# Kernel optimization log

Hardware: AMD Instinct MI355X
Metric: run time of the kernel (lower is better)

Reference implementation:

```python
import jax, jax.numpy as jnp
import numpy as np

RADIUS = 5
KS = 2 * RADIUS - 1          # kernel_size = 9
PAD = KS // 2                # 4
CENTER = RADIUS - 1          # 4 (== PAD)
EPS = 1e-10


def _offsets_and_kernel():
    # Distance kernel exactly as torch.meshgrid(indexing='ij') in the module;
    # the center entry is skipped in the loop, so drop it here.
    yy, xx = np.meshgrid(np.arange(KS), np.arange(KS), indexing='ij')
    dist = np.sqrt((xx - CENTER) ** 2 + (yy - CENTER) ** 2).astype(np.float32)
    keep = ~((yy == CENTER) & (xx == CENTER))
    return (yy[keep].astype(np.int32), xx[keep].astype(np.int32), dist[keep])


def setup_inputs() -> dict:
    key = jax.random.key(0)
    target = (jax.random.uniform(key, (5, 2048, 2048)) < 0.15).astype(jnp.float32)
    return {"target": target}


def reference(target):
    # target: [5, H, W] binary float masks
    H, W = target.shape[1], target.shape[2]
    feature_weight = jnp.sum(target, axis=0)                      # [H, W]
    combined = (feature_weight > 0).astype(jnp.float32)           # [H, W]

    padded = jnp.pad(combined, PAD, mode='edge')                  # replicate pad
    oi, oj, kv = _offsets_and_kernel()
    offs = (jnp.asarray(oi), jnp.asarray(oj), jnp.asarray(kv))

    def body(min_d, off):
        i, j, k = off
        shifted = jax.lax.dynamic_slice(padded, (i, j), (H, W))
        diff = (shifted != combined).astype(jnp.float32)
        d = jnp.where(diff > 0, k / (diff + EPS), jnp.inf)
        return jnp.minimum(min_d, d), None

    min_d, _ = jax.lax.scan(body, jnp.full((H, W), jnp.inf, jnp.float32), offs)

    contour = jnp.where(jnp.isfinite(min_d), 1.0 / (min_d + EPS), 0.0)
    w = (feature_weight + contour) ** 2
    w = (w - w.min()) / (w.max() - w.min() + EPS)
    return w * combined
```

## Files before the change

kernel.cpp:

```cpp
#include <hip/hip_runtime.h>
#include <math.h>
#include <utility>

static constexpr int HH = 2048;
static constexpr int WW = 2048;
static constexpr int NPIX = HH * WW;
static constexpr int WPR32 = WW / 32;
static constexpr int HPR = WW / 16;

template <typename F, int... Is>
__device__ __forceinline__ void sf_impl(F&& f, std::integer_sequence<int, Is...>) {
    (f(std::integral_constant<int, Is>{}), ...);
}
template <int N, typename F>
__device__ __forceinline__ void static_for(F&& f) {
    sf_impl(f, std::make_integer_sequence<int, N>{});
}

__host__ __device__ constexpr int rank_of(int d2) {
    switch (d2) {
        case 1:  return 1;  case 2:  return 2;  case 4:  return 3;
        case 5:  return 4;  case 8:  return 5;  case 9:  return 6;
        case 10: return 7;  case 13: return 8;  case 16: return 9;
        case 17: return 10; case 18: return 11; case 20: return 12;
        case 25: return 13; case 32: return 14;
    }
    return 0;
}

__device__ const int D2S[16] = {0, 1, 2, 4, 5, 8, 9, 10, 13, 16, 17, 18, 20, 25, 32, 0};

__device__ __forceinline__ unsigned long long spread8(unsigned int b) {
    unsigned long long t = (unsigned long long)b * 0x0101010101010101ull;
    t &= 0x8040201008040201ull;
    return ((t + 0x7f7f7f7f7f7f7f7full) >> 7) & 0x0101010101010101ull;
}

__global__ __launch_bounds__(256) void k_pack(const float* __restrict__ t,
                                              unsigned char* __restrict__ fw,
                                              unsigned char* __restrict__ pk) {
    const int tid = blockIdx.x * 256 + threadIdx.x;
    const int base = tid * 8;
    unsigned long long fwq = 0;
    unsigned int bits = 0;
#pragma unroll
    for (int h = 0; h < 2; ++h) {
        const int o = base + 4 * h;
        float4 a = *(const float4*)(t + 0 * NPIX + o);
        float4 b = *(const float4*)(t + 1 * NPIX + o);
        float4 c = *(const float4*)(t + 2 * NPIX + o);
        float4 d = *(const float4*)(t + 3 * NPIX + o);
        float4 e = *(const float4*)(t + 4 * NPIX + o);
        const float s0 = a.x + b.x + c.x + d.x + e.x;
        const float s1 = a.y + b.y + c.y + d.y + e.y;
        const float s2 = a.z + b.z + c.z + d.z + e.z;
        const float s3 = a.w + b.w + c.w + d.w + e.w;
        const int j = 4 * h;
        fwq |= ((unsigned long long)(int)s0) << (8 * j);
        fwq |= ((unsigned long long)(int)s1) << (8 * (j + 1));
        fwq |= ((unsigned long long)(int)s2) << (8 * (j + 2));
        fwq |= ((unsigned long long)(int)s3) << (8 * (j + 3));
        bits |= (s0 > 0.f ? 1u : 0u) << j;
        bits |= (s1 > 0.f ? 1u : 0u) << (j + 1);
        bits |= (s2 > 0.f ? 1u : 0u) << (j + 2);
        bits |= (s3 > 0.f ? 1u : 0u) << (j + 3);
    }
    *(unsigned long long*)(fw + base) = fwq;
    pk[tid] = (unsigned char)bits;
}

__global__ __launch_bounds__(1024) void k_dist(const unsigned* __restrict__ pk32,
                                               const ulonglong2* __restrict__ fw16,
                                               ulonglong2* __restrict__ code16,
                                               unsigned long long* __restrict__ obs_blk) {
    __shared__ unsigned tile[16][WPR32];
    __shared__ unsigned long long swl[16], swh[16];

    const int y0 = blockIdx.x * 8;
    {
        const int r = threadIdx.x >> 6;
        const int c = threadIdx.x & 63;
        const int gy = min(max(y0 - 4 + r, 0), HH - 1);
        tile[r][c] = pk32[gy * WPR32 + c];
    }

    const int ty = threadIdx.x >> 7;
    const int hx = threadIdx.x & 127;
    const int wx = hx >> 1;
    const int h = hx & 1;
    const int chunk = (y0 + ty) * HPR + hx;

    const ulonglong2 fv2 = fw16[chunk];

    __syncthreads();

    unsigned acc[15];
    static_for<15>([&](auto I) { acc[I.value] = 0u; });

    const unsigned Cw = tile[ty + 4][wx];
    const unsigned C = h ? (Cw >> 16) : (Cw & 0xffffu);

    static_for<9>([&](auto DY) {
        constexpr int dy = DY.value - 4;
        const int r = ty + dy + 4;
        const unsigned M = tile[r][wx];
        unsigned long long W;
        if (h == 0) {
            const unsigned P = (wx > 0) ? tile[r][wx - 1] : ((M & 1u) ? ~0u : 0u);
            W = ((unsigned long long)M << 4) | (P >> 28);
        } else {
            const unsigned N = (wx < WPR32 - 1) ? tile[r][wx + 1]
                                                : ((M >> 31) ? ~0u : 0u);
            W = ((unsigned long long)N << 20) | (M >> 12);
        }
        static_for<9>([&](auto DX) {
            constexpr int dx = DX.value - 4;
            if constexpr (!(dx == 0 && dy == 0)) {
                constexpr int rk = rank_of(dy * dy + dx * dx);
                const unsigned S = (unsigned)(W >> (4 + dx));
                acc[rk] |= S ^ C;
            }
        });
    });

    unsigned found = 0, p0 = 0, p1 = 0, p2 = 0, p3 = 0;
    static_for<14>([&](auto RI) {
        constexpr int r = RI.value + 1;
        const unsigned nw = acc[r] & ~found;
        found |= acc[r];
        if constexpr (r & 1) p0 |= nw;
        if constexpr (r & 2) p1 |= nw;
        if constexpr (r & 4) p2 |= nw;
        if constexpr (r & 8) p3 |= nw;
    });

    unsigned long long cq0 = 0, cq1 = 0;
    unsigned long long lo = 0, hi = 0;
    static_for<2>([&](auto J) {
        constexpr int j = J.value;
        const unsigned long long f = j ? fv2.y : fv2.x;
        const unsigned c0 = (p0 >> (8 * j)) & 0xff;
        const unsigned c1 = (p1 >> (8 * j)) & 0xff;
        const unsigned c2 = (p2 >> (8 * j)) & 0xff;
        const unsigned c3 = (p3 >> (8 * j)) & 0xff;
        const unsigned long long cls = spread8(c0) | (spread8(c1) << 1)
                                     | (spread8(c2) << 2) | (spread8(c3) << 3);
        const unsigned long long cq = (f << 4) | cls;
        if constexpr (j == 0) cq0 = cq; else cq1 = cq;
        static_for<8>([&](auto B) {
            constexpr int b = B.value;
            const unsigned code = (unsigned)((cq >> (8 * b)) & 0xff);
            const unsigned long long bit = 1ull << (code & 63);
            const bool ishi = (code & 64) != 0;
            lo |= ishi ? 0ull : bit;
            hi |= ishi ? bit : 0ull;
        });
    });
    code16[chunk] = make_ulonglong2(cq0, cq1);

#pragma unroll
    for (int s = 32; s > 0; s >>= 1) {
        lo |= __shfl_xor(lo, s);
        hi |= __shfl_xor(hi, s);
    }
    const int wid = threadIdx.x >> 6;
    if ((threadIdx.x & 63) == 0) { swl[wid] = lo; swh[wid] = hi; }
    __syncthreads();
    if (threadIdx.x < 64) {
        unsigned long long l2 = (threadIdx.x < 16) ? swl[threadIdx.x] : 0ull;
        unsigned long long h2 = (threadIdx.x < 16) ? swh[threadIdx.x] : 0ull;
#pragma unroll
        for (int s = 8; s > 0; s >>= 1) {
            l2 |= __shfl_xor(l2, s);
            h2 |= __shfl_xor(h2, s);
        }
        if (threadIdx.x == 0) {
            obs_blk[blockIdx.x * 2] = l2;
            obs_blk[blockIdx.x * 2 + 1] = h2;
        }
    }
}

__global__ __launch_bounds__(256) void k_out(const ulonglong2* __restrict__ code16,
                                             const unsigned long long* __restrict__ obs_blk,
                                             float* __restrict__ out) {
    __shared__ float tab[96];
    __shared__ float smn[4], smx[4];
    __shared__ unsigned long long slo[4], shi[4];

    const int tid = threadIdx.x;

    unsigned long long lo, hi;
    {
        const ulonglong2 s = ((const ulonglong2*)obs_blk)[tid];
        lo = s.x;
        hi = s.y;
#pragma unroll
        for (int s2 = 32; s2 > 0; s2 >>= 1) {
            lo |= __shfl_xor(lo, s2);
            hi |= __shfl_xor(hi, s2);
        }
        if ((tid & 63) == 0) { slo[tid >> 6] = lo; shi[tid >> 6] = hi; }
        __syncthreads();
        lo = slo[0] | slo[1] | slo[2] | slo[3];
        hi = shi[0] | shi[1] | shi[2] | shi[3];
    }

    float v = 0.f;
    bool present = false;
    if (tid < 96) {
        const int r = tid & 15;
        const float contour = (r >= 1 && r <= 14) ? 1.f / sqrtf((float)D2S[r]) : 0.f;
        const float t0 = (float)(tid >> 4) + contour;
        v = t0 * t0;
        present = (tid < 64) ? ((lo >> tid) & 1) : ((hi >> (tid - 64)) & 1);
    }
    float mnv = present ? v : INFINITY;
    float mxv = present ? v : -INFINITY;
#pragma unroll
    for (int s = 32; s > 0; s >>= 1) {
        mnv = fminf(mnv, __shfl_xor(mnv, s));
        mxv = fmaxf(mxv, __shfl_xor(mxv, s));
    }
    if ((tid & 63) == 0) { smn[tid >> 6] = mnv; smx[tid >> 6] = mxv; }
    __syncthreads();
    const float mn = fminf(fminf(smn[0], smn[1]), fminf(smn[2], smn[3]));
    const float mx = fmaxf(fmaxf(smx[0], smx[1]), fmaxf(smx[2], smx[3]));
    const float inv = 1.f / (mx - mn + 1e-10f);
    if (tid < 96) tab[tid] = (tid >= 16) ? (v - mn) * inv : 0.f;
    __syncthreads();

    const int t = blockIdx.x * 256 + tid;
    const ulonglong2 cq = code16[t];
    float4 v0, v1, v2, v3;
    v0.x = tab[(cq.x >> 0) & 0xff];  v0.y = tab[(cq.x >> 8) & 0xff];
    v0.z = tab[(cq.x >> 16) & 0xff]; v0.w = tab[(cq.x >> 24) & 0xff];
    v1.x = tab[(cq.x >> 32) & 0xff]; v1.y = tab[(cq.x >> 40) & 0xff];
    v1.z = tab[(cq.x >> 48) & 0xff]; v1.w = tab[(cq.x >> 56) & 0xff];
    v2.x = tab[(cq.y >> 0) & 0xff];  v2.y = tab[(cq.y >> 8) & 0xff];
    v2.z = tab[(cq.y >> 16) & 0xff]; v2.w = tab[(cq.y >> 24) & 0xff];
    v3.x = tab[(cq.y >> 32) & 0xff]; v3.y = tab[(cq.y >> 40) & 0xff];
    v3.z = tab[(cq.y >> 48) & 0xff]; v3.w = tab[(cq.y >> 56) & 0xff];
    const int ob = t * 16;
    *(float4*)(out + ob + 0)  = v0;
    *(float4*)(out + ob + 4)  = v1;
    *(float4*)(out + ob + 8)  = v2;
    *(float4*)(out + ob + 12) = v3;
}

extern "C" void kernel_launch(void* const* d_in, const int* in_sizes, int n_in,
                              void* d_out, int out_size, void* d_ws, size_t ws_size,
                              hipStream_t stream) {
    const float* target = (const float*)d_in[0];
    float* out = (float*)d_out;

    unsigned char* fw = (unsigned char*)d_ws;
    unsigned char* pk = fw + NPIX;
    unsigned char* code = pk + NPIX / 8;
    unsigned long long* obs_blk = (unsigned long long*)(code + NPIX);

    k_pack<<<NPIX / 8 / 256, 256, 0, stream>>>(target, fw, pk);

    k_dist<<<HH / 8, 1024, 0, stream>>>(
        (const unsigned*)pk, (const ulonglong2*)fw,
        (ulonglong2*)code, obs_blk);

    k_out<<<NPIX / 16 / 256, 256, 0, stream>>>(
        (const ulonglong2*)code, obs_blk, out);
}
```

Measured before the change: 36.81 us.

## Fuse packing and distance passes into one 2D-tiled kernel with halo recompute

Merges the separate pack and distance kernels into one kernel working on 256x64 tiles. Each tile sums the five masks straight from global memory, including a 4-pixel halo, builds the bit-packed mask with wave ballots and keeps the per-pixel feature weight in shared memory. This removes the global round trip for the intermediate feature-weight and packed-mask buffers and one kernel launch. In exchange it re-reads halo pixels, uses scalar float loads instead of float4, and launches only 256 blocks of 512 threads, which may limit how many memory requests are in flight.

Result: slower. 45.25 us (+22.9%).

```diff
diff --git a/kernel.cpp b/kernel.cpp
--- a/kernel.cpp
+++ b/kernel.cpp
@@ -5,8 +5,11 @@
 static constexpr int HH = 2048;
 static constexpr int WW = 2048;
 static constexpr int NPIX = HH * WW;
-static constexpr int WPR32 = WW / 32;
 static constexpr int HPR = WW / 16;
+static constexpr int TW = 256;
+static constexpr int TH = 64;
+static constexpr int GX = WW / TW;
+static constexpr int GY = HH / TH;
 
 template <typename F, int... Is>
 __device__ __forceinline__ void sf_impl(F&& f, std::integer_sequence<int, Is...>) {
@@ -36,146 +39,140 @@
     return ((t + 0x7f7f7f7f7f7f7f7full) >> 7) & 0x0101010101010101ull;
 }
 
-__global__ __launch_bounds__(256) void k_pack(const float* __restrict__ t,
-                                              unsigned char* __restrict__ fw,
-                                              unsigned char* __restrict__ pk) {
-    const int tid = blockIdx.x * 256 + threadIdx.x;
-    const int base = tid * 8;
-    unsigned long long fwq = 0;
-    unsigned int bits = 0;
-#pragma unroll
-    for (int h = 0; h < 2; ++h) {
-        const int o = base + 4 * h;
-        float4 a = *(const float4*)(t + 0 * NPIX + o);
-        float4 b = *(const float4*)(t + 1 * NPIX + o);
-        float4 c = *(const float4*)(t + 2 * NPIX + o);
-        float4 d = *(const float4*)(t + 3 * NPIX + o);
-        float4 e = *(const float4*)(t + 4 * NPIX + o);
-        const float s0 = a.x + b.x + c.x + d.x + e.x;
-        const float s1 = a.y + b.y + c.y + d.y + e.y;
-        const float s2 = a.z + b.z + c.z + d.z + e.z;
-        const float s3 = a.w + b.w + c.w + d.w + e.w;
-        const int j = 4 * h;
-        fwq |= ((unsigned long long)(int)s0) << (8 * j);
-        fwq |= ((unsigned long long)(int)s1) << (8 * (j + 1));
-        fwq |= ((unsigned long long)(int)s2) << (8 * (j + 2));
-        fwq |= ((unsigned long long)(int)s3) << (8 * (j + 3));
-        bits |= (s0 > 0.f ? 1u : 0u) << j;
-        bits |= (s1 > 0.f ? 1u : 0u) << (j + 1);
-        bits |= (s2 > 0.f ? 1u : 0u) << (j + 2);
-        bits |= (s3 > 0.f ? 1u : 0u) << (j + 3);
-    }
-    *(unsigned long long*)(fw + base) = fwq;
-    pk[tid] = (unsigned char)bits;
-}
-
-__global__ __launch_bounds__(1024) void k_dist(const unsigned* __restrict__ pk32,
-                                               const ulonglong2* __restrict__ fw16,
-                                               ulonglong2* __restrict__ code16,
-                                               unsigned long long* __restrict__ obs_blk) {
-    __shared__ unsigned tile[16][WPR32];
-    __shared__ unsigned long long swl[16], swh[16];
-
-    const int y0 = blockIdx.x * 8;
-    {
-        const int r = threadIdx.x >> 6;
-        const int c = threadIdx.x & 63;
-        const int gy = min(max(y0 - 4 + r, 0), HH - 1);
-        tile[r][c] = pk32[gy * WPR32 + c];
-    }
-
-    const int ty = threadIdx.x >> 7;
-    const int hx = threadIdx.x & 127;
-    const int wx = hx >> 1;
-    const int h = hx & 1;
-    const int chunk = (y0 + ty) * HPR + hx;
-
-    const ulonglong2 fv2 = fw16[chunk];
-
-    __syncthreads();
-
-    unsigned acc[15];
-    static_for<15>([&](auto I) { acc[I.value] = 0u; });
-
-    const unsigned Cw = tile[ty + 4][wx];
-    const unsigned C = h ? (Cw >> 16) : (Cw & 0xffffu);
-
-    static_for<9>([&](auto DY) {
-        constexpr int dy = DY.value - 4;
-        const int r = ty + dy + 4;
-        const unsigned M = tile[r][wx];
-        unsigned long long W;
-        if (h == 0) {
-            const unsigned P = (wx > 0) ? tile[r][wx - 1] : ((M & 1u) ? ~0u : 0u);
-            W = ((unsigned long long)M << 4) | (P >> 28);
-        } else {
-            const unsigned N = (wx < WPR32 - 1) ? tile[r][wx + 1]
-                                                : ((M >> 31) ? ~0u : 0u);
-            W = ((unsigned long long)N << 20) | (M >> 12);
-        }
-        static_for<9>([&](auto DX) {
-            constexpr int dx = DX.value - 4;
-            if constexpr (!(dx == 0 && dy == 0)) {
-                constexpr int rk = rank_of(dy * dy + dx * dx);
-                const unsigned S = (unsigned)(W >> (4 + dx));
-                acc[rk] |= S ^ C;
+__global__ __launch_bounds__(512) void k_packdist(const float* __restrict__ t,
+                                                  ulonglong2* __restrict__ code16,
+                                                  unsigned long long* __restrict__ obs_blk) {
+    __shared__ unsigned pkt[TH + 8][9];
+    __shared__ unsigned char fwt[TH][TW];
+    __shared__ unsigned long long swl[8], swh[8];
+
+    const int bx = blockIdx.x & (GX - 1);
+    const int by = blockIdx.x >> 3;
+    const int tx0 = bx * TW, ty0 = by * TH;
+    const int wid = threadIdx.x >> 6, lane = threadIdx.x & 63;
+
+#pragma unroll 5
+    for (int it = wid * 45; it < wid * 45 + 45; ++it) {
+        const int r = it / 5;
+        const int s = it - 5 * r;
+        const bool active = (s < 4) | (lane < 8);
+        const int c = (s < 4) ? (64 * s - 4 + lane) : (252 + lane);
+        const int gy = min(max(ty0 + r - 4, 0), HH - 1);
+        const int gx = min(max(tx0 + c, 0), WW - 1);
+        float s5 = 0.f;
+        if (active) {
+            const int o = gy * WW + gx;
+            s5 = t[o] + t[NPIX + o] + t[2 * NPIX + o] + t[3 * NPIX + o]
+               + t[4 * NPIX + o];
+        }
+        const unsigned long long bal = __ballot(active && (s5 > 0.f));
+        if (lane == 0) {
+            if (s < 4) {
+                pkt[r][2 * s]     = (unsigned)bal;
+                pkt[r][2 * s + 1] = (unsigned)(bal >> 32);
+            } else {
+                pkt[r][8] = (unsigned)bal;
             }
+        }
+        const int rr = r - 4;
+        if (active && rr >= 0 && rr < TH && c >= 0 && c < TW)
+            fwt[rr][c] = (unsigned char)(int)s5;
+    }
+    __syncthreads();
+
+    unsigned long long obl = 0, obh = 0;
+#pragma unroll
+    for (int k = 0; k < 2; ++k) {
+        const int ch = threadIdx.x + k * 512;
+        const int rr = ch >> 4;
+        const int cx = ch & 15;
+        const int x0 = cx * 16;
+        const int w0 = x0 >> 5;
+        const int sh = x0 & 31;
+
+        unsigned acc[15];
+        static_for<15>([&](auto I) { acc[I.value] = 0u; });
+
+        const unsigned long long Wc =
+            ((unsigned long long)pkt[rr + 4][w0]
+           | ((unsigned long long)pkt[rr + 4][w0 + 1] << 32)) >> sh;
+        const unsigned C = (unsigned)(Wc >> 4);
+
+        static_for<9>([&](auto DY) {
+            constexpr int dyi = DY.value;
+            constexpr int dy = dyi - 4;
+            const unsigned long long W = (dyi == 4) ? Wc :
+                (((unsigned long long)pkt[rr + dyi][w0]
+                | ((unsigned long long)pkt[rr + dyi][w0 + 1] << 32)) >> sh);
+            static_for<9>([&](auto DX) {
+                constexpr int dx = DX.value - 4;
+                if constexpr (!(dx == 0 && dy == 0)) {
+                    constexpr int rk = rank_of(dy * dy + dx * dx);
+                    const unsigned S = (unsigned)(W >> (4 + dx));
+                    acc[rk] |= S ^ C;
+                }
+            });
         });
-    });
-
-    unsigned found = 0, p0 = 0, p1 = 0, p2 = 0, p3 = 0;
-    static_for<14>([&](auto RI) {
-        constexpr int r = RI.value + 1;
-        const unsigned nw = acc[r] & ~found;
-        found |= acc[r];
-        if constexpr (r & 1) p0 |= nw;
-        if constexpr (r & 2) p1 |= nw;
-        if constexpr (r & 4) p2 |= nw;
-        if constexpr (r & 8) p3 |= nw;
-    });
-
-    unsigned long long cq0 = 0, cq1 = 0;
-    unsigned long long lo = 0, hi = 0;
-    static_for<2>([&](auto J) {
-        constexpr int j = J.value;
-        const unsigned long long f = j ? fv2.y : fv2.x;
-        const unsigned c0 = (p0 >> (8 * j)) & 0xff;
-        const unsigned c1 = (p1 >> (8 * j)) & 0xff;
-        const unsigned c2 = (p2 >> (8 * j)) & 0xff;
-        const unsigned c3 = (p3 >> (8 * j)) & 0xff;
-        const unsigned long long cls = spread8(c0) | (spread8(c1) << 1)
-                                     | (spread8(c2) << 2) | (spread8(c3) << 3);
-        const unsigned long long cq = (f << 4) | cls;
-        if constexpr (j == 0) cq0 = cq; else cq1 = cq;
-        static_for<8>([&](auto B) {
-            constexpr int b = B.value;
-            const unsigned code = (unsigned)((cq >> (8 * b)) & 0xff);
-            const unsigned long long bit = 1ull << (code & 63);
-            const bool ishi = (code & 64) != 0;
-            lo |= ishi ? 0ull : bit;
-            hi |= ishi ? bit : 0ull;
+
+        unsigned found = 0, p0 = 0, p1 = 0, p2 = 0, p3 = 0;
+        static_for<14>([&](auto RI) {
+            constexpr int r = RI.value + 1;
+            const unsigned nw = acc[r] & ~found;
+            found |= acc[r];
+            if constexpr (r & 1) p0 |= nw;
+            if constexpr (r & 2) p1 |= nw;
+            if constexpr (r & 4) p2 |= nw;
+            if constexpr (r & 8) p3 |= nw;
         });
-    });
-    code16[chunk] = make_ulonglong2(cq0, cq1);
+
+        const uint4 fvw = *(const uint4*)&fwt[rr][x0];
+        const unsigned long long fv0 =
+            (unsigned long long)fvw.x | ((unsigned long long)fvw.y << 32);
+        const unsigned long long fv1 =
+            (unsigned long long)fvw.z | ((unsigned long long)fvw.w << 32);
+
+        unsigned long long cq0 = 0, cq1 = 0;
+        static_for<2>([&](auto J) {
+            constexpr int j = J.value;
+            const unsigned long long f = j ? fv1 : fv0;
+            const unsigned c0 = (p0 >> (8 * j)) & 0xff;
+            const unsigned c1 = (p1 >> (8 * j)) & 0xff;
+            const unsigned c2 = (p2 >> (8 * j)) & 0xff;
+            const unsigned c3 = (p3 >> (8 * j)) & 0xff;
+            const unsigned long long cls = spread8(c0) | (spread8(c1) << 1)
+                                         | (spread8(c2) << 2) | (spread8(c3) << 3);
+            const unsigned long long cq = (f << 4) | cls;
+            if constexpr (j == 0) cq0 = cq; else cq1 = cq;
+            static_for<8>([&](auto B) {
+                constexpr int b = B.value;
+                const unsigned code = (unsigned)((cq >> (8 * b)) & 0xff);
+                const unsigned long long bit = 1ull << (code & 63);
+                const bool ishi = (code & 64) != 0;
+                obl |= ishi ? 0ull : bit;
+                obh |= ishi ? bit : 0ull;
+            });
+        });
+        const int gchunk = (ty0 + rr) * HPR + bx * (TW / 16) + cx;
+        code16[gchunk] = make_ulonglong2(cq0, cq1);
+    }
 
 #pragma unroll
     for (int s = 32; s > 0; s >>= 1) {
-        lo |= __shfl_xor(lo, s);
-        hi |= __shfl_xor(hi, s);
-    }
-    const int wid = threadIdx.x >> 6;
-    if ((threadIdx.x & 63) == 0) { swl[wid] = lo; swh[wid] = hi; }
+        obl |= __shfl_xor(obl, s);
+        obh |= __shfl_xor(obh, s);
+    }
+    if (lane == 0) { swl[wid] = obl; swh[wid] = obh; }
     __syncthreads();
     if (threadIdx.x < 64) {
-        unsigned long long l2 = (threadIdx.x < 16) ? swl[threadIdx.x] : 0ull;
-        unsigned long long h2 = (threadIdx.x < 16) ? swh[threadIdx.x] : 0ull;
-#pragma unroll
-        for (int s = 8; s > 0; s >>= 1) {
+        unsigned long long l2 = (threadIdx.x < 8) ? swl[threadIdx.x] : 0ull;
+        unsigned long long h2 = (threadIdx.x < 8) ? swh[threadIdx.x] : 0ull;
+#pragma unroll
+        for (int s = 4; s > 0; s >>= 1) {
             l2 |= __shfl_xor(l2, s);
             h2 |= __shfl_xor(h2, s);
         }
         if (threadIdx.x == 0) {
-            obs_blk[blockIdx.x * 2] = l2;
+            obs_blk[blockIdx.x * 2]     = l2;
             obs_blk[blockIdx.x * 2 + 1] = h2;
         }
     }
@@ -254,16 +251,11 @@
     const float* target = (const float*)d_in[0];
     float* out = (float*)d_out;
 
-    unsigned char* fw = (unsigned char*)d_ws;
-    unsigned char* pk = fw + NPIX;
-    unsigned char* code = pk + NPIX / 8;
+    unsigned char* code = (unsigned char*)d_ws;
     unsigned long long* obs_blk = (unsigned long long*)(code + NPIX);
 
-    k_pack<<<NPIX / 8 / 256, 256, 0, stream>>>(target, fw, pk);
-
-    k_dist<<<HH / 8, 1024, 0, stream>>>(
-        (const unsigned*)pk, (const ulonglong2*)fw,
-        (ulonglong2*)code, obs_blk);
+    k_packdist<<<GX * GY, 512, 0, stream>>>(
+        target, (ulonglong2*)code, obs_blk);
 
     k_out<<<NPIX / 16 / 256, 256, 0, stream>>>(
         (const ulonglong2*)code, obs_blk, out);
```
